# Performance work log

Hardware: AMD Instinct MI355X
Metric: run time of the kernel (lower is better)

The kernel has to match this reference:

```python
import jax, jax.numpy as jnp
import numpy as np

ACTION_NS = [3, 3, 2, 4, 24]        # forward_back, left_right, jump, sneak_sprint, attack_...
RANGE_STARTS = [6, 8, 10, 11, 14]   # action_ranges starts (indices 0..5 are commit + camera ops)
N_ACTIONS = 37
LOGIT_DIM = 36
MIN_DELTA = 0.5 / 2**3
MAX_STEP = 20
MAX_CAMSTEP = 6
B, NUM_INPUT, HIDDEN = 32768, 1024, 2048
D_IN = NUM_INPUT + 4 + LOGIT_DIM


def setup_inputs():
    key = jax.random.key(0)
    ks = jax.random.split(key, 12)
    inp = {
        "fc_input": jax.random.normal(ks[0], (B, NUM_INPUT), jnp.float32),
        "camera": jax.random.normal(ks[1], (B, 2), jnp.float32),
        "rand_u": jax.random.uniform(ks[2], (B,), jnp.float32),
        "W1": (jax.random.normal(ks[3], (D_IN, HIDDEN), jnp.float32) / np.sqrt(D_IN)).astype(jnp.float32),
        "b1": jnp.zeros((HIDDEN,), jnp.float32),
        "W2": (jax.random.normal(ks[4], (HIDDEN, N_ACTIONS), jnp.float32) / np.sqrt(HIDDEN)).astype(jnp.float32),
        "b2": jnp.zeros((N_ACTIONS,), jnp.float32),
    }
    names = ["act_fb", "act_lr", "act_jp", "act_ss", "act_atk"]
    for i, (nm, n) in enumerate(zip(names, ACTION_NS)):
        inp[nm] = jax.random.randint(ks[5 + i], (B,), 0, n, jnp.int32)
    return inp


def _discretize_scan(camera, acts):
    # Faithful jax version of the 20-step no_grad target/input construction loop.
    nB = camera.shape[0]
    cam0, cam1 = camera[:, 0], camera[:, 1]

    def step(carry, _):
        ac, delta, rdac, dch, cam_steps, committed, norm = carry
        oh = [jax.nn.one_hot(r, n, dtype=jnp.float32) for r, n in zip(rdac, ACTION_NS)]
        inp_vec = jnp.concatenate([ac] + oh + [delta[:, None], dch.astype(jnp.float32)[:, None]], axis=1)  # [B,40]
        norm = norm + (~committed).astype(jnp.float32)
        commit = ((jnp.abs(cam0) < 1e-5) & (jnp.abs(cam1) < 1e-5)) | (cam_steps >= MAX_CAMSTEP)
        for r, a in zip(rdac, acts):
            commit = commit & (r == a)
        dac = jnp.zeros((nB,), jnp.int32)
        modified = commit
        new_rdac = []
        for r, a, rs in zip(rdac, acts, RANGE_STARTS):
            disc = (~modified) & (r != a)
            dac = jnp.where(disc & (a == 0), r - 1 + rs, jnp.where(disc, a - 1 + rs, dac))
            new_rdac.append(jnp.where(disc, a, r))
            modified = modified | disc
        d2 = delta * 2.0
        # NOTE: original torch code compares cam[:,1] against ac[:,0]; bug preserved.
        dmask = (~modified) & (~dch) & ((jnp.abs(cam0 - ac[:, 0]) > d2) | (jnp.abs(cam1 - ac[:, 0]) > d2))
        dac = jnp.where(dmask, 5, dac)
        delta = jnp.where(dmask, jnp.clip(d2, -0.5, 0.5), delta)
        modified = modified | dmask
        sx = jnp.where(cam0 < ac[:, 0], -1.0, 1.0)
        sy = jnp.where(cam1 < ac[:, 1], -1.0, 1.0)
        quad = jnp.where(sx < 0, jnp.where(sy < 0, 1, 3), jnp.where(sy < 0, 2, 4)).astype(jnp.int32)
        dac = jnp.where(~modified, quad, dac)
        move = jnp.stack([sx, sy], axis=1) * delta[:, None]
        ac = jnp.where((~modified)[:, None], ac + move, ac)
        delta = jnp.where(~modified, delta * 0.5, delta)
        dch = dch | (~modified)
        cam_steps = cam_steps + (~modified).astype(jnp.int32)
        committed = committed | commit
        return (ac, delta, tuple(new_rdac), dch, cam_steps, committed, norm), (inp_vec, dac)

    init = (jnp.zeros((nB, 2), jnp.float32),
            jnp.full((nB,), MIN_DELTA, jnp.float32),
            tuple(jnp.zeros((nB,), jnp.int32) for _ in ACTION_NS),
            jnp.zeros((nB,), bool),
            jnp.zeros((nB,), jnp.int32),
            jnp.zeros((nB,), bool),
            jnp.zeros((nB,), jnp.float32))
    carry, (all_inputs, all_dacs) = jax.lax.scan(step, init, None, length=MAX_STEP)
    return all_inputs, all_dacs, carry[-1]  # [T,B,40], [T,B], norm [B]


def reference(fc_input, camera, rand_u, W1, b1, W2, b2, act_fb, act_lr, act_jp, act_ss, act_atk):
    acts = (act_fb, act_lr, act_jp, act_ss, act_atk)
    all_inputs, all_dacs, norm = _discretize_scan(camera, acts)
    rand_sam = jnp.minimum((rand_u * norm).astype(jnp.int32), MAX_STEP - 1)  # sample an uncommitted step
    idx = jnp.arange(fc_input.shape[0])
    sel = jax.lax.stop_gradient(all_inputs[rand_sam, idx])  # [B,40]
    tgt = jax.lax.stop_gradient(all_dacs[rand_sam, idx])    # [B]
    x = jnp.concatenate([fc_input, sel], axis=1)
    h = x @ W1 + b1
    h = h * jax.nn.sigmoid(h)  # swish
    logits = h @ W2 + b2
    logp = jax.nn.log_softmax(logits, axis=-1)
    loss = -jnp.take_along_axis(logp, tgt[:, None], axis=1)[:, 0]  # per-sample CE (reduction='none')
    return loss
```

## Files before the change

kernel.cpp:

```cpp
#include <hip/hip_runtime.h>
#include <hip/hip_bf16.h>
#include <stdint.h>

#define B_ROWS 32768
#define NUM_IN 1024
#define D_PAD2 1088
#define HID    2048
#define NPAD   64

typedef __attribute__((ext_vector_type(8))) short bf16x8;
typedef __attribute__((ext_vector_type(4))) float f32x4;
typedef unsigned short ushort_t;

__device__ __forceinline__ unsigned short f2bf(float f){
  union { float f; uint32_t u; } x; x.f = f;
  uint32_t u = x.u;
  return (unsigned short)((u + 0x7FFFu + ((u >> 16) & 1u)) >> 16);
}

__device__ __forceinline__ void gload16(const void* g, void* l){
  __builtin_amdgcn_global_load_lds((const __attribute__((address_space(1))) void*)g,
                                   (__attribute__((address_space(3))) void*)l, 16, 0, 0);
}

__device__ __forceinline__ int disc_step(
    float cam0, float cam1, const int a[5],
    float& ac0, float& ac1, float& delta,
    int r[5], bool& dch, int& cam_steps, bool& committed, float& norm)
{
  const int RS[5] = {6, 8, 10, 11, 14};
  norm += committed ? 0.0f : 1.0f;
  bool commit = ((fabsf(cam0) < 1e-5f) && (fabsf(cam1) < 1e-5f)) || (cam_steps >= 6);
  #pragma unroll
  for (int i = 0; i < 5; ++i) commit = commit && (r[i] == a[i]);
  int dac = 0;
  bool modified = commit;
  #pragma unroll
  for (int i = 0; i < 5; ++i){
    bool disc = (!modified) && (r[i] != a[i]);
    if (disc){
      dac = (a[i] == 0) ? (r[i] - 1 + RS[i]) : (a[i] - 1 + RS[i]);
      r[i] = a[i];
      modified = true;
    }
  }
  float d2 = delta * 2.0f;
  bool dmask = (!modified) && (!dch) &&
               ((fabsf(cam0 - ac0) > d2) || (fabsf(cam1 - ac0) > d2));
  if (dmask){ dac = 5; delta = fminf(d2, 0.5f); modified = true; }
  if (!modified){
    float sx = (cam0 < ac0) ? -1.0f : 1.0f;
    float sy = (cam1 < ac1) ? -1.0f : 1.0f;
    dac = (sx < 0.0f) ? ((sy < 0.0f) ? 1 : 3) : ((sy < 0.0f) ? 2 : 4);
    ac0 += sx * delta; ac1 += sy * delta;
    delta *= 0.5f;
    dch = true;
    cam_steps += 1;
  }
  committed = committed || commit;
  return dac;
}

__global__ void k_prep(const float* __restrict__ fc, const float* __restrict__ W1,
                       const float* __restrict__ W2,
                       const float* __restrict__ camera, const float* __restrict__ rand_u,
                       const int* __restrict__ afb, const int* __restrict__ alr,
                       const int* __restrict__ ajp, const int* __restrict__ ass,
                       const int* __restrict__ aat,
                       unsigned short* __restrict__ xb, unsigned short* __restrict__ w1t,
                       unsigned short* __restrict__ w2t, int* __restrict__ tgt)
{
  __shared__ float lt[64][65];
  const int b = blockIdx.x;
  const int tid = threadIdx.x;
  if (b < 16384){
    int gid = b * 256 + tid;
    int row = gid >> 7;
    int c   = gid & 127;
    const float4* p = (const float4*)(fc + (size_t)row * NUM_IN + c * 8);
    float4 f0 = p[0], f1 = p[1];
    uint4 pk;
    pk.x = (uint32_t)f2bf(f0.x) | ((uint32_t)f2bf(f0.y) << 16);
    pk.y = (uint32_t)f2bf(f0.z) | ((uint32_t)f2bf(f0.w) << 16);
    pk.z = (uint32_t)f2bf(f1.x) | ((uint32_t)f2bf(f1.y) << 16);
    pk.w = (uint32_t)f2bf(f1.z) | ((uint32_t)f2bf(f1.w) << 16);
    *(uint4*)(xb + (size_t)row * D_PAD2 + c * 8) = pk;
    return;
  }
  if (b < 16928){
    const int bi = b - 16384;
    const int kt = bi % 17, nt = bi / 17;
    const int k0 = kt * 64, n0 = nt * 64;
    const int c = tid & 63, rq = tid >> 6;
    #pragma unroll
    for (int rr = 0; rr < 16; ++rr){
      const int r = rr * 4 + rq;
      const int k = k0 + r;
      lt[r][c] = (k < 1064) ? W1[(size_t)k * HID + n0 + c] : 0.0f;
    }
    __syncthreads();
    #pragma unroll
    for (int rr = 0; rr < 16; ++rr){
      const int r = rr * 4 + rq;
      w1t[(size_t)(n0 + r) * D_PAD2 + k0 + c] = f2bf(lt[c][r]);
    }
    return;
  }
  if (b < 17440){
    int idx = (b - 16928) * 256 + tid;
    int n = idx >> 11;
    int k = idx & (HID - 1);
    float v = (n < 37) ? W2[(size_t)k * 37 + n] : 0.0f;
    w2t[idx] = f2bf(v);
    return;
  }
  int row = (b - 17440) * 256 + tid;
  float cam0 = camera[2*row], cam1 = camera[2*row + 1];
  int a[5] = { afb[row], alr[row], ajp[row], ass[row], aat[row] };

  float ac0 = 0.f, ac1 = 0.f, delta = 0.0625f, norm = 0.f;
  int r[5] = {0,0,0,0,0};
  bool dch = false, committed = false; int cam_steps = 0;
  for (int t = 0; t < 20; ++t)
    disc_step(cam0, cam1, a, ac0, ac1, delta, r, dch, cam_steps, committed, norm);

  int rs = (int)(rand_u[row] * norm);
  if (rs > 19) rs = 19;
  if (rs < 0) rs = 0;

  ac0 = 0.f; ac1 = 0.f; delta = 0.0625f; norm = 0.f;
  r[0]=r[1]=r[2]=r[3]=r[4]=0; dch = false; committed = false; cam_steps = 0;
  for (int t = 0; t < rs; ++t)
    disc_step(cam0, cam1, a, ac0, ac1, delta, r, dch, cam_steps, committed, norm);

  float vec[40];
  #pragma unroll
  for (int j = 0; j < 40; ++j) vec[j] = 0.0f;
  vec[0] = ac0; vec[1] = ac1;
  const int offs[5] = {2, 5, 8, 10, 14};
  #pragma unroll
  for (int i = 0; i < 5; ++i) vec[offs[i] + r[i]] = 1.0f;
  vec[38] = delta; vec[39] = dch ? 1.0f : 0.0f;

  int dac = disc_step(cam0, cam1, a, ac0, ac1, delta, r, dch, cam_steps, committed, norm);
  tgt[row] = dac;

  unsigned short* o = xb + (size_t)row * D_PAD2 + NUM_IN;
  #pragma unroll
  for (int j = 0; j < 40; ++j) o[j] = f2bf(vec[j]);
  #pragma unroll
  for (int j = 40; j < 64; ++j) o[j] = 0;
}

#define LDS_A0 0
#define LDS_A1 16384
#define LDS_B0 32768
#define LDS_B1 49152

#define STAGE(G, REG, ROW0, KT, HALF) do { \
    const ushort_t* s0_ = (G) + (size_t)((ROW0) + (HALF)*128 + srow) * D_PAD2 + ((KT) << 6) + scol; \
    gload16(s0_, lds + (REG) + (HALF)*8192 + t*8); \
    gload16(s0_ + (size_t)64 * D_PAD2, lds + (REG) + (HALF)*8192 + 4096 + t*8); \
  } while(0)

#define LDA_(BUF, MH) do { \
    _Pragma("unroll") for (int mi_ = 0; mi_ < 4; ++mi_) \
    _Pragma("unroll") for (int kk_ = 0; kk_ < 2; ++kk_) \
      aR[mi_][kk_] = *(const bf16x8*)(aBk[kk_] + (BUF)*32768 + ((MH)*64 + mi_*16)*128); \
  } while(0)

#define LDB_(BUF, NH, BR) do { \
    _Pragma("unroll") for (int ni_ = 0; ni_ < 2; ++ni_) \
    _Pragma("unroll") for (int kk_ = 0; kk_ < 2; ++kk_) \
      BR[ni_][kk_] = *(const bf16x8*)(bBk[kk_] + (BUF)*32768 + ((NH)*32 + ni_*16)*128); \
  } while(0)

#define MMA(MH, NH, BR) do { \
    __builtin_amdgcn_s_setprio(1); \
    _Pragma("unroll") for (int mi_ = 0; mi_ < 4; ++mi_) \
    _Pragma("unroll") for (int ni_ = 0; ni_ < 2; ++ni_) \
    _Pragma("unroll") for (int kk_ = 0; kk_ < 2; ++kk_) \
      acc[(MH)*4+mi_][(NH)*2+ni_] = __builtin_amdgcn_mfma_f32_16x16x32_bf16( \
          aR[mi_][kk_], BR[ni_][kk_], acc[(MH)*4+mi_][(NH)*2+ni_], 0, 0, 0); \
    __builtin_amdgcn_s_setprio(0); \
  } while(0)

#define BAR() __builtin_amdgcn_s_barrier()
#define LGKM0()    asm volatile("s_waitcnt lgkmcnt(0)" ::: "memory")
#define LGKM8()    asm volatile("s_waitcnt lgkmcnt(8)" ::: "memory")
#define WAIT_VM4() asm volatile("s_waitcnt vmcnt(4)" ::: "memory")
#define WAIT_VM0() asm volatile("s_waitcnt vmcnt(0)" ::: "memory")

__global__ __launch_bounds__(512, 2) void k_gemm1(const ushort_t* __restrict__ xb,
                                                  const ushort_t* __restrict__ w1t,
                                                  const ushort_t* __restrict__ w2t,
                                                  const float* __restrict__ b1,
                                                  float* __restrict__ pbuf)
{
  __shared__ ushort_t lds[65536];
  const int t = threadIdx.x;
  const int lane = t & 63;
  const int wid = t >> 6, wm = wid >> 2, wn = wid & 3;
  const int lr = lane & 15, lg = lane >> 4;

  const int bid = blockIdx.x;
  const int swz = (bid & 7) * 128 + (bid >> 3);
  const int brow = (swz >> 3) << 8;
  const int bcol = (swz & 7) << 8;

  const int srow = t >> 3;
  const int scol = ((t & 7) ^ (srow & 7)) << 3;

  const int axor = lr & 7;
  const int arow_base = wm*128 + lr;
  const int brow_base = wn*64 + lr;

  const char* aBk[2];
  const char* bBk[2];
  aBk[0] = (const char*)lds + arow_base*128 + (((0*4+lg)^axor) << 4);
  aBk[1] = (const char*)lds + arow_base*128 + (((1*4+lg)^axor) << 4);
  bBk[0] = (const char*)lds + 65536 + brow_base*128 + (((0*4+lg)^axor) << 4);
  bBk[1] = (const char*)lds + 65536 + brow_base*128 + (((1*4+lg)^axor) << 4);

  f32x4 acc[8][4] = {};
  bf16x8 aR[4][2], bR0[2][2], bR1[2][2];

  STAGE(xb,  LDS_A0, brow, 0, 0);  STAGE(xb,  LDS_A0, brow, 0, 1);
  STAGE(w1t, LDS_B0, bcol, 0, 0);  STAGE(w1t, LDS_B0, bcol, 0, 1);
  STAGE(w1t, LDS_B1, bcol, 1, 0);  STAGE(w1t, LDS_B1, bcol, 1, 1);
  WAIT_VM4();
  BAR();

  for (int i = 0; i < 8; ++i){
    const int c1 = 2*i + 1;
    const int n0 = 2*i + 2;
    const int n1 = (2*i + 3 <= 16) ? 2*i + 3 : 16;

    LDA_(0, 0); LDB_(0, 0, bR0);
    STAGE(xb, LDS_A1, brow, c1, 0);
    LGKM8();
    BAR(); LGKM0();
    MMA(0, 0, bR0);
    BAR();
    LDB_(0, 1, bR1);
    STAGE(xb, LDS_A1, brow, c1, 1);
    BAR(); LGKM0();
    MMA(0, 1, bR1);
    BAR();
    LDA_(0, 1);
    STAGE(w1t, LDS_B0, bcol, n0, 0);
    BAR(); LGKM0();
    MMA(1, 0, bR0);
    BAR();
    STAGE(w1t, LDS_B0, bcol, n0, 1);
    WAIT_VM4();
    BAR();
    MMA(1, 1, bR1);
    BAR();
    LDA_(1, 0); LDB_(1, 0, bR0);
    STAGE(xb, LDS_A0, brow, n0, 0);
    LGKM8();
    BAR(); LGKM0();
    MMA(0, 0, bR0);
    BAR();
    LDB_(1, 1, bR1);
    STAGE(xb, LDS_A0, brow, n0, 1);
    BAR(); LGKM0();
    MMA(0, 1, bR1);
    BAR();
    LDA_(1, 1);
    STAGE(w1t, LDS_B1, bcol, n1, 0);
    BAR(); LGKM0();
    MMA(1, 0, bR0);
    BAR();
    STAGE(w1t, LDS_B1, bcol, n1, 1);
    WAIT_VM4();
    BAR();
    MMA(1, 1, bR1);
    BAR();
  }

  LDA_(0, 0); LDB_(0, 0, bR0); LDB_(0, 1, bR1);
  LGKM0();
  MMA(0, 0, bR0); MMA(0, 1, bR1);
  LDA_(0, 1);
  LGKM0();
  MMA(1, 0, bR0); MMA(1, 1, bR1);

  bf16x8 w2fA[4][4];
  #pragma unroll
  for (int ks = 0; ks < 4; ++ks)
    #pragma unroll
    for (int ni = 0; ni < 4; ++ni)
      w2fA[ks][ni] = *(const bf16x8*)(w2t + (size_t)(ni*16 + lr) * HID + bcol + ks*32 + lg*8);

  WAIT_VM0();
  BAR();

  float b1v[4];
  #pragma unroll
  for (int ni = 0; ni < 4; ++ni) b1v[ni] = b1[bcol + wn*64 + ni*16 + lr];

  #pragma unroll
  for (int mi = 0; mi < 8; ++mi){
    #pragma unroll
    for (int ni = 0; ni < 4; ++ni){
      const int col = wn*64 + ni*16 + lr;
      #pragma unroll
      for (int i2 = 0; i2 < 4; ++i2){
        const int row = wm*128 + mi*16 + lg*4 + i2;
        float v = acc[mi][ni][i2] + b1v[ni];
        float s = v / (1.0f + __expf(-v));
        const int chunk = (col >> 3) ^ (row & 7);
        lds[row*256 + chunk*8 + (col & 7)] = f2bf(s);
      }
    }
  }
  __syncthreads();

  bf16x8 w2fB[4][4];
  #pragma unroll
  for (int ks = 0; ks < 4; ++ks)
    #pragma unroll
    for (int ni = 0; ni < 4; ++ni)
      w2fB[ks][ni] = *(const bf16x8*)(w2t + (size_t)(ni*16 + lr) * HID + bcol + (ks+4)*32 + lg*8);

  const int rb = wid * 32;
  f32x4 acc2[2][4] = {};
  #pragma unroll
  for (int ks = 0; ks < 8; ++ks){
    bf16x8 a2[2];
    #pragma unroll
    for (int m = 0; m < 2; ++m){
      const int row = rb + m*16 + lr;
      a2[m] = *(const bf16x8*)(lds + row*256 + (((ks*4+lg) ^ (lr & 7)) << 3));
    }
    #pragma unroll
    for (int m = 0; m < 2; ++m)
      #pragma unroll
      for (int ni = 0; ni < 4; ++ni)
        acc2[m][ni] = __builtin_amdgcn_mfma_f32_16x16x32_bf16(
            a2[m], (ks < 4) ? w2fA[ks & 3][ni] : w2fB[ks & 3][ni], acc2[m][ni], 0, 0, 0);
  }

  const int cb = bcol >> 8;
  #pragma unroll
  for (int m = 0; m < 2; ++m)
    #pragma unroll
    for (int ni = 0; ni < 4; ++ni)
      #pragma unroll
      for (int i2 = 0; i2 < 4; ++i2){
        const int r = brow + rb + m*16 + lg*4 + i2;
        pbuf[((size_t)cb << 21) + ((size_t)r << 6) + ni*16 + lr] = acc2[m][ni][i2];
      }
}

__global__ __launch_bounds__(256) void k_red(const float* __restrict__ pbuf,
                                             const float* __restrict__ b2,
                                             const int* __restrict__ tgt,
                                             float* __restrict__ loss)
{
  const int lane = threadIdx.x & 63, w = threadIdx.x >> 6;
  const int row0 = blockIdx.x * 128 + w * 32;
  const float bias = (lane < 37) ? b2[lane] : 0.0f;
  for (int i = 0; i < 32; ++i){
    const int r = row0 + i;
    float s = 0.0f;
    #pragma unroll
    for (int cb = 0; cb < 8; ++cb)
      s += pbuf[((size_t)cb << 21) + ((size_t)r << 6) + lane];
    float x = (lane < 37) ? (s + bias) : -1e30f;
    float m = x;
    #pragma unroll
    for (int off = 1; off < 64; off <<= 1) m = fmaxf(m, __shfl_xor(m, off, 64));
    float e = __expf(x - m);
    float se = e;
    #pragma unroll
    for (int off = 1; off < 64; off <<= 1) se += __shfl_xor(se, off, 64);
    const int tg = tgt[r];
    const float pick = __shfl(x, tg, 64);
    if (lane == 0) loss[r] = m + __logf(se) - pick;
  }
}

extern "C" void kernel_launch(void* const* d_in, const int* in_sizes, int n_in,
                              void* d_out, int out_size, void* d_ws, size_t ws_size,
                              hipStream_t stream)
{
  (void)in_sizes; (void)n_in; (void)out_size; (void)ws_size;
  const float* fc  = (const float*)d_in[0];
  const float* cam = (const float*)d_in[1];
  const float* ru  = (const float*)d_in[2];
  const float* W1  = (const float*)d_in[3];
  const float* b1  = (const float*)d_in[4];
  const float* W2  = (const float*)d_in[5];
  const float* b2  = (const float*)d_in[6];
  const int* afb = (const int*)d_in[7];
  const int* alr = (const int*)d_in[8];
  const int* ajp = (const int*)d_in[9];
  const int* ass = (const int*)d_in[10];
  const int* aat = (const int*)d_in[11];
  float* loss = (float*)d_out;

  char* ws = (char*)d_ws;
  unsigned short* xb  = (unsigned short*)(ws);
  unsigned short* w1t = (unsigned short*)(ws + 71303168);
  unsigned short* w2t = (unsigned short*)(ws + 75759616);
  int*            tgt = (int*)           (ws + 76021760);
  float*          pbuf= (float*)         (ws + 76152832);

  k_prep<<<17568, 256, 0, stream>>>(fc, W1, W2, cam, ru, afb, alr, ajp, ass, aat,
                                    xb, w1t, w2t, tgt);
  k_gemm1<<<(B_ROWS/256) * (HID/256), 512, 0, stream>>>(xb, w1t, w2t, b1, pbuf);
  k_red  <<<B_ROWS / 128, 256, 0, stream>>>(pbuf, b2, tgt, loss);
}
```

Baseline: 269.0 us.

## Use 1024-thread blocks with 16 waves splitting the 256x256 tile

Doubles the GEMM workgroup from 8 to 16 waves, so each wave owns a 64x64 sub-tile instead of 128x64. This halves the accumulator and A-fragment registers per wave. Staging now issues one 16-byte global-to-LDS load per thread per half-tile, and the vmcnt waits and load order are reworked to match. The second GEMM now streams W2 fragments from global memory each k-step instead of preloading them into registers. The aim is more resident waves to hide latency, at the cost of more barrier participants and repeated W2 global loads.

```diff
diff --git a/kernel.cpp b/kernel.cpp
--- a/kernel.cpp
+++ b/kernel.cpp
@@ -157,16 +157,15 @@
 #define LDS_B0 32768
 #define LDS_B1 49152
 
-#define STAGE(G, REG, ROW0, KT, HALF) do { \
-    const ushort_t* s0_ = (G) + (size_t)((ROW0) + (HALF)*128 + srow) * D_PAD2 + ((KT) << 6) + scol; \
-    gload16(s0_, lds + (REG) + (HALF)*8192 + t*8); \
-    gload16(s0_ + (size_t)64 * D_PAD2, lds + (REG) + (HALF)*8192 + 4096 + t*8); \
+#define STAGE1(G, REG, ROW0, KT, S) do { \
+    const ushort_t* s0_ = (G) + (size_t)((ROW0) + (S)*128 + srow) * D_PAD2 + ((KT) << 6) + scol; \
+    gload16(s0_, lds + (REG) + (S)*8192 + t*8); \
   } while(0)
 
 #define LDA_(BUF, MH) do { \
-    _Pragma("unroll") for (int mi_ = 0; mi_ < 4; ++mi_) \
+    _Pragma("unroll") for (int mi_ = 0; mi_ < 2; ++mi_) \
     _Pragma("unroll") for (int kk_ = 0; kk_ < 2; ++kk_) \
-      aR[mi_][kk_] = *(const bf16x8*)(aBk[kk_] + (BUF)*32768 + ((MH)*64 + mi_*16)*128); \
+      aR[mi_][kk_] = *(const bf16x8*)(aBk[kk_] + (BUF)*32768 + ((MH)*32 + mi_*16)*128); \
   } while(0)
 
 #define LDB_(BUF, NH, BR) do { \
@@ -177,30 +176,31 @@
 
 #define MMA(MH, NH, BR) do { \
     __builtin_amdgcn_s_setprio(1); \
-    _Pragma("unroll") for (int mi_ = 0; mi_ < 4; ++mi_) \
+    _Pragma("unroll") for (int mi_ = 0; mi_ < 2; ++mi_) \
     _Pragma("unroll") for (int ni_ = 0; ni_ < 2; ++ni_) \
     _Pragma("unroll") for (int kk_ = 0; kk_ < 2; ++kk_) \
-      acc[(MH)*4+mi_][(NH)*2+ni_] = __builtin_amdgcn_mfma_f32_16x16x32_bf16( \
-          aR[mi_][kk_], BR[ni_][kk_], acc[(MH)*4+mi_][(NH)*2+ni_], 0, 0, 0); \
+      acc[(MH)*2+mi_][(NH)*2+ni_] = __builtin_amdgcn_mfma_f32_16x16x32_bf16( \
+          aR[mi_][kk_], BR[ni_][kk_], acc[(MH)*2+mi_][(NH)*2+ni_], 0, 0, 0); \
     __builtin_amdgcn_s_setprio(0); \
   } while(0)
 
 #define BAR() __builtin_amdgcn_s_barrier()
 #define LGKM0()    asm volatile("s_waitcnt lgkmcnt(0)" ::: "memory")
-#define LGKM8()    asm volatile("s_waitcnt lgkmcnt(8)" ::: "memory")
-#define WAIT_VM4() asm volatile("s_waitcnt vmcnt(4)" ::: "memory")
+#define WAIT_VM2() asm volatile("s_waitcnt vmcnt(2)" ::: "memory")
+#define WAIT_VM3() asm volatile("s_waitcnt vmcnt(3)" ::: "memory")
 #define WAIT_VM0() asm volatile("s_waitcnt vmcnt(0)" ::: "memory")
 
-__global__ __launch_bounds__(512, 2) void k_gemm1(const ushort_t* __restrict__ xb,
-                                                  const ushort_t* __restrict__ w1t,
-                                                  const ushort_t* __restrict__ w2t,
-                                                  const float* __restrict__ b1,
-                                                  float* __restrict__ pbuf)
+__global__ __launch_bounds__(1024, 4) void k_gemm1(const ushort_t* __restrict__ xb,
+                                                   const ushort_t* __restrict__ w1t,
+                                                   const ushort_t* __restrict__ w2t,
+                                                   const float* __restrict__ b1,
+                                                   float* __restrict__ pbuf)
 {
   __shared__ ushort_t lds[65536];
   const int t = threadIdx.x;
   const int lane = t & 63;
-  const int wid = t >> 6, wm = wid >> 2, wn = wid & 3;
+  const int wid = t >> 6;
+  const int wm = wid >> 2, wn = wid & 3;
   const int lr = lane & 15, lg = lane >> 4;
 
   const int bid = blockIdx.x;
@@ -212,69 +212,65 @@
   const int scol = ((t & 7) ^ (srow & 7)) << 3;
 
   const int axor = lr & 7;
-  const int arow_base = wm*128 + lr;
-  const int brow_base = wn*64 + lr;
-
   const char* aBk[2];
   const char* bBk[2];
-  aBk[0] = (const char*)lds + arow_base*128 + (((0*4+lg)^axor) << 4);
-  aBk[1] = (const char*)lds + arow_base*128 + (((1*4+lg)^axor) << 4);
-  bBk[0] = (const char*)lds + 65536 + brow_base*128 + (((0*4+lg)^axor) << 4);
-  bBk[1] = (const char*)lds + 65536 + brow_base*128 + (((1*4+lg)^axor) << 4);
-
-  f32x4 acc[8][4] = {};
-  bf16x8 aR[4][2], bR0[2][2], bR1[2][2];
-
-  STAGE(xb,  LDS_A0, brow, 0, 0);  STAGE(xb,  LDS_A0, brow, 0, 1);
-  STAGE(w1t, LDS_B0, bcol, 0, 0);  STAGE(w1t, LDS_B0, bcol, 0, 1);
-  STAGE(w1t, LDS_B1, bcol, 1, 0);  STAGE(w1t, LDS_B1, bcol, 1, 1);
-  WAIT_VM4();
+  aBk[0] = (const char*)lds + (wm*64 + lr)*128 + (((0*4+lg)^axor) << 4);
+  aBk[1] = (const char*)lds + (wm*64 + lr)*128 + (((1*4+lg)^axor) << 4);
+  bBk[0] = (const char*)lds + 65536 + (wn*64 + lr)*128 + (((0*4+lg)^axor) << 4);
+  bBk[1] = (const char*)lds + 65536 + (wn*64 + lr)*128 + (((1*4+lg)^axor) << 4);
+
+  f32x4 acc[4][4] = {};
+  bf16x8 aR[2][2], bR0[2][2], bR1[2][2];
+
+  STAGE1(xb,  LDS_A0, brow, 0, 0);  STAGE1(xb,  LDS_A0, brow, 0, 1);
+  STAGE1(w1t, LDS_B0, bcol, 0, 0);  STAGE1(w1t, LDS_B0, bcol, 0, 1);
+  STAGE1(w1t, LDS_B1, bcol, 1, 0);  STAGE1(w1t, LDS_B1, bcol, 1, 1);
+  STAGE1(xb,  LDS_A1, brow, 1, 0);
+  WAIT_VM3();
   BAR();
 
   for (int i = 0; i < 8; ++i){
-    const int c1 = 2*i + 1;
+    const int t1 = 2*i + 1;
     const int n0 = 2*i + 2;
     const int n1 = (2*i + 3 <= 16) ? 2*i + 3 : 16;
 
     LDA_(0, 0); LDB_(0, 0, bR0);
-    STAGE(xb, LDS_A1, brow, c1, 0);
-    LGKM8();
+    STAGE1(xb, LDS_A1, brow, t1, 1);
     BAR(); LGKM0();
     MMA(0, 0, bR0);
     BAR();
     LDB_(0, 1, bR1);
-    STAGE(xb, LDS_A1, brow, c1, 1);
     BAR(); LGKM0();
     MMA(0, 1, bR1);
     BAR();
     LDA_(0, 1);
-    STAGE(w1t, LDS_B0, bcol, n0, 0);
+    STAGE1(w1t, LDS_B0, bcol, n0, 0);
     BAR(); LGKM0();
     MMA(1, 0, bR0);
     BAR();
-    STAGE(w1t, LDS_B0, bcol, n0, 1);
-    WAIT_VM4();
+    STAGE1(w1t, LDS_B0, bcol, n0, 1);
+    WAIT_VM2();
     BAR();
     MMA(1, 1, bR1);
     BAR();
     LDA_(1, 0); LDB_(1, 0, bR0);
-    STAGE(xb, LDS_A0, brow, n0, 0);
-    LGKM8();
+    STAGE1(xb, LDS_A0, brow, n0, 0);
     BAR(); LGKM0();
     MMA(0, 0, bR0);
     BAR();
     LDB_(1, 1, bR1);
-    STAGE(xb, LDS_A0, brow, n0, 1);
+    STAGE1(xb, LDS_A0, brow, n0, 1);
     BAR(); LGKM0();
     MMA(0, 1, bR1);
     BAR();
     LDA_(1, 1);
-    STAGE(w1t, LDS_B1, bcol, n1, 0);
+    STAGE1(w1t, LDS_B1, bcol, n1, 0);
     BAR(); LGKM0();
     MMA(1, 0, bR0);
     BAR();
-    STAGE(w1t, LDS_B1, bcol, n1, 1);
-    WAIT_VM4();
+    STAGE1(w1t, LDS_B1, bcol, n1, 1);
+    STAGE1(xb, LDS_A1, brow, n1, 0);
+    WAIT_VM3();
     BAR();
     MMA(1, 1, bR1);
     BAR();
@@ -287,13 +283,6 @@
   LGKM0();
   MMA(1, 0, bR0); MMA(1, 1, bR1);
 
-  bf16x8 w2fA[4][4];
-  #pragma unroll
-  for (int ks = 0; ks < 4; ++ks)
-    #pragma unroll
-    for (int ni = 0; ni < 4; ++ni)
-      w2fA[ks][ni] = *(const bf16x8*)(w2t + (size_t)(ni*16 + lr) * HID + bcol + ks*32 + lg*8);
-
   WAIT_VM0();
   BAR();
 
@@ -302,13 +291,13 @@
   for (int ni = 0; ni < 4; ++ni) b1v[ni] = b1[bcol + wn*64 + ni*16 + lr];
 
   #pragma unroll
-  for (int mi = 0; mi < 8; ++mi){
+  for (int mi = 0; mi < 4; ++mi){
     #pragma unroll
     for (int ni = 0; ni < 4; ++ni){
       const int col = wn*64 + ni*16 + lr;
       #pragma unroll
       for (int i2 = 0; i2 < 4; ++i2){
-        const int row = wm*128 + mi*16 + lg*4 + i2;
+        const int row = wm*64 + mi*16 + lg*4 + i2;
         float v = acc[mi][ni][i2] + b1v[ni];
         float s = v / (1.0f + __expf(-v));
         const int chunk = (col >> 3) ^ (row & 7);
@@ -318,41 +307,28 @@
   }
   __syncthreads();
 
-  bf16x8 w2fB[4][4];
-  #pragma unroll
-  for (int ks = 0; ks < 4; ++ks)
+  const int rb = wid * 16;
+  f32x4 acc2[4] = {};
+  #pragma unroll
+  for (int ks = 0; ks < 8; ++ks){
+    bf16x8 a2 = *(const bf16x8*)(lds + (rb + lr)*256 + (((ks*4+lg) ^ (lr & 7)) << 3));
+    bf16x8 b2f[4];
     #pragma unroll
     for (int ni = 0; ni < 4; ++ni)
-      w2fB[ks][ni] = *(const bf16x8*)(w2t + (size_t)(ni*16 + lr) * HID + bcol + (ks+4)*32 + lg*8);
-
-  const int rb = wid * 32;
-  f32x4 acc2[2][4] = {};
-  #pragma unroll
-  for (int ks = 0; ks < 8; ++ks){
-    bf16x8 a2[2];
-    #pragma unroll
-    for (int m = 0; m < 2; ++m){
-      const int row = rb + m*16 + lr;
-      a2[m] = *(const bf16x8*)(lds + row*256 + (((ks*4+lg) ^ (lr & 7)) << 3));
-    }
-    #pragma unroll
-    for (int m = 0; m < 2; ++m)
-      #pragma unroll
-      for (int ni = 0; ni < 4; ++ni)
-        acc2[m][ni] = __builtin_amdgcn_mfma_f32_16x16x32_bf16(
-            a2[m], (ks < 4) ? w2fA[ks & 3][ni] : w2fB[ks & 3][ni], acc2[m][ni], 0, 0, 0);
+      b2f[ni] = *(const bf16x8*)(w2t + (size_t)(ni*16 + lr) * HID + bcol + ks*32 + lg*8);
+    #pragma unroll
+    for (int ni = 0; ni < 4; ++ni)
+      acc2[ni] = __builtin_amdgcn_mfma_f32_16x16x32_bf16(a2, b2f[ni], acc2[ni], 0, 0, 0);
   }
 
   const int cb = bcol >> 8;
   #pragma unroll
-  for (int m = 0; m < 2; ++m)
-    #pragma unroll
-    for (int ni = 0; ni < 4; ++ni)
-      #pragma unroll
-      for (int i2 = 0; i2 < 4; ++i2){
-        const int r = brow + rb + m*16 + lg*4 + i2;
-        pbuf[((size_t)cb << 21) + ((size_t)r << 6) + ni*16 + lr] = acc2[m][ni][i2];
-      }
+  for (int ni = 0; ni < 4; ++ni)
+    #pragma unroll
+    for (int i2 = 0; i2 < 4; ++i2){
+      const int r = brow + rb + lg*4 + i2;
+      pbuf[((size_t)cb << 21) + ((size_t)r << 6) + ni*16 + lr] = acc2[ni][i2];
+    }
 }
 
 __global__ __launch_bounds__(256) void k_red(const float* __restrict__ pbuf,
@@ -411,6 +387,6 @@
 
   k_prep<<<17568, 256, 0, stream>>>(fc, W1, W2, cam, ru, afb, alr, ajp, ass, aat,
                                     xb, w1t, w2t, tgt);
-  k_gemm1<<<(B_ROWS/256) * (HID/256), 512, 0, stream>>>(xb, w1t, w2t, b1, pbuf);
+  k_gemm1<<<(B_ROWS/256) * (HID/256), 1024, 0, stream>>>(xb, w1t, w2t, b1, pbuf);
   k_red  <<<B_ROWS / 128, 256, 0, stream>>>(pbuf, b2, tgt, loss);
 }
```

New measurement: 350.6 us. 1.3x slower.

## Pre-pack W1 in MFMA fragment order and load B operands directly to registers

Applied to the files above, without the earlier changes.

The prep kernel now writes W1 pre-swizzled into per-wave MFMA fragment layout, so the GEMM loads B fragments straight from global memory into registers instead of staging them through LDS. The A tile uses a triple-buffered LDS ring with a simpler single-barrier-per-k-step fully unrolled loop. This cuts LDS traffic and barriers for B, at the cost of more global/L2 reads per wave (no block-level B sharing), more register pressure, and possible exposed global-load latency.

```diff
diff --git a/kernel.cpp b/kernel.cpp
--- a/kernel.cpp
+++ b/kernel.cpp
@@ -67,7 +67,7 @@
                        const int* __restrict__ afb, const int* __restrict__ alr,
                        const int* __restrict__ ajp, const int* __restrict__ ass,
                        const int* __restrict__ aat,
-                       unsigned short* __restrict__ xb, unsigned short* __restrict__ w1t,
+                       unsigned short* __restrict__ xb, unsigned short* __restrict__ w1p,
                        unsigned short* __restrict__ w2t, int* __restrict__ tgt)
 {
   __shared__ float lt[64][65];
@@ -91,6 +91,7 @@
     const int bi = b - 16384;
     const int kt = bi % 17, nt = bi / 17;
     const int k0 = kt * 64, n0 = nt * 64;
+    const int cgrp = nt >> 2, wn = nt & 3;
     const int c = tid & 63, rq = tid >> 6;
     #pragma unroll
     for (int rr = 0; rr < 16; ++rr){
@@ -100,9 +101,22 @@
     }
     __syncthreads();
     #pragma unroll
-    for (int rr = 0; rr < 16; ++rr){
-      const int r = rr * 4 + rq;
-      w1t[(size_t)(n0 + r) * D_PAD2 + k0 + c] = f2bf(lt[c][r]);
+    for (int s = 0; s < 2; ++s){
+      const int idx = s * 256 + tid;
+      const int ln = idx & 63, q = idx >> 6;
+      const int lr2 = ln & 15, lg2 = ln >> 4;
+      const int np = (q >> 2) * 32 + ((q >> 1) & 1) * 16 + lr2;
+      const int kx = (q & 1) * 32 + lg2 * 8;
+      uint4 pk;
+      uint32_t w[4];
+      #pragma unroll
+      for (int e = 0; e < 4; ++e){
+        unsigned short lo = f2bf(lt[kx + 2*e][np]);
+        unsigned short hi = f2bf(lt[kx + 2*e + 1][np]);
+        w[e] = (uint32_t)lo | ((uint32_t)hi << 16);
+      }
+      pk.x = w[0]; pk.y = w[1]; pk.z = w[2]; pk.w = w[3];
+      *(uint4*)(w1p + (((size_t)cgrp*17 + kt) << 14) + (wn << 12) + q*512 + ln*8) = pk;
     }
     return;
   }
@@ -152,47 +166,42 @@
   for (int j = 40; j < 64; ++j) o[j] = 0;
 }
 
-#define LDS_A0 0
-#define LDS_A1 16384
-#define LDS_B0 32768
-#define LDS_B1 49152
-
-#define STAGE(G, REG, ROW0, KT, HALF) do { \
-    const ushort_t* s0_ = (G) + (size_t)((ROW0) + (HALF)*128 + srow) * D_PAD2 + ((KT) << 6) + scol; \
+
+#define STAGE(REG, KT, HALF) do { \
+    const ushort_t* s0_ = xb + (size_t)(brow + (HALF)*128 + srow) * D_PAD2 + ((KT) << 6) + scol; \
     gload16(s0_, lds + (REG) + (HALF)*8192 + t*8); \
     gload16(s0_ + (size_t)64 * D_PAD2, lds + (REG) + (HALF)*8192 + 4096 + t*8); \
   } while(0)
 
-#define LDA_(BUF, MH) do { \
+#define LDA_T(BO, MH) do { \
     _Pragma("unroll") for (int mi_ = 0; mi_ < 4; ++mi_) \
     _Pragma("unroll") for (int kk_ = 0; kk_ < 2; ++kk_) \
-      aR[mi_][kk_] = *(const bf16x8*)(aBk[kk_] + (BUF)*32768 + ((MH)*64 + mi_*16)*128); \
+      aR[mi_][kk_] = *(const bf16x8*)(aBk[kk_] + (BO) + (((MH)*64 + mi_*16)*128)); \
   } while(0)
 
-#define LDB_(BUF, NH, BR) do { \
+#define GLBH(BANK, KT, NH) do { \
+    const ushort_t* bp_ = w1p + (((size_t)cgrp*17 + (KT)) << 14) + (wn << 12) + ((NH)*4)*512 + lane*8; \
     _Pragma("unroll") for (int ni_ = 0; ni_ < 2; ++ni_) \
     _Pragma("unroll") for (int kk_ = 0; kk_ < 2; ++kk_) \
-      BR[ni_][kk_] = *(const bf16x8*)(bBk[kk_] + (BUF)*32768 + ((NH)*32 + ni_*16)*128); \
+      BANK[ni_][kk_] = *(const bf16x8*)(bp_ + (ni_*2 + kk_)*512); \
   } while(0)
 
-#define MMA(MH, NH, BR) do { \
+#define MMA(MH, NH, BH) do { \
     __builtin_amdgcn_s_setprio(1); \
     _Pragma("unroll") for (int mi_ = 0; mi_ < 4; ++mi_) \
     _Pragma("unroll") for (int ni_ = 0; ni_ < 2; ++ni_) \
     _Pragma("unroll") for (int kk_ = 0; kk_ < 2; ++kk_) \
       acc[(MH)*4+mi_][(NH)*2+ni_] = __builtin_amdgcn_mfma_f32_16x16x32_bf16( \
-          aR[mi_][kk_], BR[ni_][kk_], acc[(MH)*4+mi_][(NH)*2+ni_], 0, 0, 0); \
+          aR[mi_][kk_], BH[ni_][kk_], acc[(MH)*4+mi_][(NH)*2+ni_], 0, 0, 0); \
     __builtin_amdgcn_s_setprio(0); \
   } while(0)
 
 #define BAR() __builtin_amdgcn_s_barrier()
-#define LGKM0()    asm volatile("s_waitcnt lgkmcnt(0)" ::: "memory")
-#define LGKM8()    asm volatile("s_waitcnt lgkmcnt(8)" ::: "memory")
 #define WAIT_VM4() asm volatile("s_waitcnt vmcnt(4)" ::: "memory")
 #define WAIT_VM0() asm volatile("s_waitcnt vmcnt(0)" ::: "memory")
 
 __global__ __launch_bounds__(512, 2) void k_gemm1(const ushort_t* __restrict__ xb,
-                                                  const ushort_t* __restrict__ w1t,
+                                                  const ushort_t* __restrict__ w1p,
                                                   const ushort_t* __restrict__ w2t,
                                                   const float* __restrict__ b1,
                                                   float* __restrict__ pbuf)
@@ -207,85 +216,47 @@
   const int swz = (bid & 7) * 128 + (bid >> 3);
   const int brow = (swz >> 3) << 8;
   const int bcol = (swz & 7) << 8;
+  const int cgrp = bcol >> 8;
 
   const int srow = t >> 3;
   const int scol = ((t & 7) ^ (srow & 7)) << 3;
 
   const int axor = lr & 7;
-  const int arow_base = wm*128 + lr;
-  const int brow_base = wn*64 + lr;
-
   const char* aBk[2];
-  const char* bBk[2];
-  aBk[0] = (const char*)lds + arow_base*128 + (((0*4+lg)^axor) << 4);
-  aBk[1] = (const char*)lds + arow_base*128 + (((1*4+lg)^axor) << 4);
-  bBk[0] = (const char*)lds + 65536 + brow_base*128 + (((0*4+lg)^axor) << 4);
-  bBk[1] = (const char*)lds + 65536 + brow_base*128 + (((1*4+lg)^axor) << 4);
+  aBk[0] = (const char*)lds + (wm*128 + lr)*128 + (((0*4+lg)^axor) << 4);
+  aBk[1] = (const char*)lds + (wm*128 + lr)*128 + (((1*4+lg)^axor) << 4);
 
   f32x4 acc[8][4] = {};
-  bf16x8 aR[4][2], bR0[2][2], bR1[2][2];
-
-  STAGE(xb,  LDS_A0, brow, 0, 0);  STAGE(xb,  LDS_A0, brow, 0, 1);
-  STAGE(w1t, LDS_B0, bcol, 0, 0);  STAGE(w1t, LDS_B0, bcol, 0, 1);
-  STAGE(w1t, LDS_B1, bcol, 1, 0);  STAGE(w1t, LDS_B1, bcol, 1, 1);
+  bf16x8 aR[4][2];
+  bf16x8 bH0[2][2], bH1[2][2];
+
+  STAGE(0, 0, 0);  STAGE(0, 0, 1);
+  GLBH(bH0, 0, 0); GLBH(bH1, 0, 1);
+  STAGE(16384, 1, 0);  STAGE(16384, 1, 1);
   WAIT_VM4();
   BAR();
 
-  for (int i = 0; i < 8; ++i){
-    const int c1 = 2*i + 1;
-    const int n0 = 2*i + 2;
-    const int n1 = (2*i + 3 <= 16) ? 2*i + 3 : 16;
-
-    LDA_(0, 0); LDB_(0, 0, bR0);
-    STAGE(xb, LDS_A1, brow, c1, 0);
-    LGKM8();
-    BAR(); LGKM0();
-    MMA(0, 0, bR0);
-    BAR();
-    LDB_(0, 1, bR1);
-    STAGE(xb, LDS_A1, brow, c1, 1);
-    BAR(); LGKM0();
-    MMA(0, 1, bR1);
-    BAR();
-    LDA_(0, 1);
-    STAGE(w1t, LDS_B0, bcol, n0, 0);
-    BAR(); LGKM0();
-    MMA(1, 0, bR0);
-    BAR();
-    STAGE(w1t, LDS_B0, bcol, n0, 1);
+  #pragma unroll
+  for (int tt = 0; tt < 17; ++tt){
+    const int cbuf = (tt % 3) * 32768;
+    const int sbo  = ((tt + 2) % 3) * 16384;
+    const int st   = (tt + 2 <= 16) ? tt + 2 : 16;
+    const int nk   = (tt + 1 <= 16) ? tt + 1 : 16;
+
+    LDA_T(cbuf, 0);
+    MMA(0, 0, bH0);
+    MMA(0, 1, bH1);
+    LDA_T(cbuf, 1);
+    MMA(1, 0, bH0);
+    GLBH(bH0, nk, 0);
+    MMA(1, 1, bH1);
+    GLBH(bH1, nk, 1);
+    __builtin_amdgcn_sched_barrier(0);
+    STAGE(sbo, st, 0);
+    STAGE(sbo, st, 1);
     WAIT_VM4();
     BAR();
-    MMA(1, 1, bR1);
-    BAR();
-    LDA_(1, 0); LDB_(1, 0, bR0);
-    STAGE(xb, LDS_A0, brow, n0, 0);
-    LGKM8();
-    BAR(); LGKM0();
-    MMA(0, 0, bR0);
-    BAR();
-    LDB_(1, 1, bR1);
-    STAGE(xb, LDS_A0, brow, n0, 1);
-    BAR(); LGKM0();
-    MMA(0, 1, bR1);
-    BAR();
-    LDA_(1, 1);
-    STAGE(w1t, LDS_B1, bcol, n1, 0);
-    BAR(); LGKM0();
-    MMA(1, 0, bR0);
-    BAR();
-    STAGE(w1t, LDS_B1, bcol, n1, 1);
-    WAIT_VM4();
-    BAR();
-    MMA(1, 1, bR1);
-    BAR();
-  }
-
-  LDA_(0, 0); LDB_(0, 0, bR0); LDB_(0, 1, bR1);
-  LGKM0();
-  MMA(0, 0, bR0); MMA(0, 1, bR1);
-  LDA_(0, 1);
-  LGKM0();
-  MMA(1, 0, bR0); MMA(1, 1, bR1);
+  }
 
   bf16x8 w2fA[4][4];
   #pragma unroll
@@ -343,7 +314,7 @@
             a2[m], (ks < 4) ? w2fA[ks & 3][ni] : w2fB[ks & 3][ni], acc2[m][ni], 0, 0, 0);
   }
 
-  const int cb = bcol >> 8;
+  const int cb = cgrp;
   #pragma unroll
   for (int m = 0; m < 2; ++m)
     #pragma unroll
@@ -404,13 +375,13 @@
 
   char* ws = (char*)d_ws;
   unsigned short* xb  = (unsigned short*)(ws);
-  unsigned short* w1t = (unsigned short*)(ws + 71303168);
+  unsigned short* w1p = (unsigned short*)(ws + 71303168);
   unsigned short* w2t = (unsigned short*)(ws + 75759616);
   int*            tgt = (int*)           (ws + 76021760);
   float*          pbuf= (float*)         (ws + 76152832);
 
   k_prep<<<17568, 256, 0, stream>>>(fc, W1, W2, cam, ru, afb, alr, ajp, ass, aat,
-                                    xb, w1t, w2t, tgt);
-  k_gemm1<<<(B_ROWS/256) * (HID/256), 512, 0, stream>>>(xb, w1t, w2t, b1, pbuf);
+                                    xb, w1p, w2t, tgt);
+  k_gemm1<<<(B_ROWS/256) * (HID/256), 512, 0, stream>>>(xb, w1p, w2t, b1, pbuf);
   k_red  <<<B_ROWS / 128, 256, 0, stream>>>(pbuf, b2, tgt, loss);
 }
```

New measurement: 275.3 us. 2.3% more time.
